# Optimization experiments

Hardware: AMD Instinct MI355X
Metric: run time of the kernel (lower is better)

## Reference

```python
import jax, jax.numpy as jnp
import numpy as np

T, B, H = 2048, 8, 1024


def setup_inputs() -> dict:
    key = jax.random.key(0)
    ks = jax.random.split(key, 4)
    scale = 1.0 / np.sqrt(H)
    x = jax.random.normal(ks[0], (T, B, H), dtype=jnp.float32)
    W_q = jax.random.normal(ks[1], (H, H), dtype=jnp.float32) * scale
    b_q = jnp.zeros((H,), dtype=jnp.float32)
    beta_raw = jax.random.normal(ks[2], (H,), dtype=jnp.float32)
    W_fc = jax.random.normal(ks[3], (H, H), dtype=jnp.float32) * scale
    b_fc = jnp.zeros((H,), dtype=jnp.float32)
    return {"x": x, "W_q": W_q, "b_q": b_q, "beta_raw": beta_raw,
            "W_fc": W_fc, "b_fc": b_fc}


def reference(x, W_q, b_q, beta_raw, W_fc, b_fc):
    # Per-neuron learned leak in (0,1)
    beta = jax.nn.sigmoid(beta_raw)  # (H,)
    # Input (q) projection: (T,B,H) @ (H,H)^T
    q = jnp.einsum('tbh,oh->tbo', x, W_q) + b_q  # (T,B,H)
    # Leaky integration m_t = beta * m_{t-1} + q_t as an associative scan over T
    a = jnp.broadcast_to(beta, q.shape)  # (T,B,H)

    def combine(c1, c2):
        a1, m1 = c1
        a2, m2 = c2
        return (a1 * a2, a2 * m1 + m2)

    _, m = jax.lax.associative_scan(combine, (a, q), axis=0)  # (T,B,H)
    # Linear + ReLU
    h = jnp.einsum('tbh,oh->tbo', m, W_fc) + b_fc
    return jax.nn.relu(h)
```

## Files before the change

kernel.cpp:

```cpp
#include <hip/hip_runtime.h>
#include <stdint.h>

typedef unsigned short u16;
typedef __bf16 bf16x8 __attribute__((ext_vector_type(8)));
typedef float f32x4 __attribute__((ext_vector_type(4)));

__device__ __forceinline__ u16 f2bf(float f) {
  union { float f; uint32_t u; } x; x.f = f;
  uint32_t u = x.u;
  u += 0x7fffu + ((u >> 16) & 1u);
  return (u16)(u >> 16);
}
__device__ __forceinline__ float bf2f(uint32_t lo16) {
  union { uint32_t u; float f; } x; x.u = lo16 << 16; return x.f;
}

__device__ __forceinline__ void async_load16(const u16* g, u16* l) {
  __builtin_amdgcn_global_load_lds(
      (const __attribute__((address_space(1))) void*)g,
      (__attribute__((address_space(3))) void*)l,
      16, 0, 0);
}

__global__ __launch_bounds__(256) void prep_all(const float* __restrict__ x,
                                                const float* __restrict__ Wq,
                                                const float* __restrict__ Wfc,
                                                const float* __restrict__ braw,
                                                u16* __restrict__ xb,
                                                u16* __restrict__ wqb,
                                                u16* __restrict__ wfcb,
                                                float* __restrict__ beta) {
  int gid = blockIdx.x * 256 + threadIdx.x;
  if (gid < 1024) beta[gid] = 1.0f / (1.0f + expf(-braw[gid]));
  if (gid < 131072) {
    const int HH = 1024 * 1024;
    int i = gid * 16;
    const float* src = (i < HH) ? (Wq + i) : (Wfc + (i - HH));
    u16* dst = (i < HH) ? (wqb + i) : (wfcb + (i - HH));
#pragma unroll
    for (int c = 0; c < 4; c++) {
      float4 v = *(const float4*)(src + c * 4);
      ushort4 o = {f2bf(v.x), f2bf(v.y), f2bf(v.z), f2bf(v.w)};
      *(ushort4*)(dst + c * 4) = o;
    }
  }
  {
    int i = gid * 8;
    float4 a = *(const float4*)(x + i);
    float4 b = *(const float4*)(x + i + 4);
    ushort4 o0 = {f2bf(a.x), f2bf(a.y), f2bf(a.z), f2bf(a.w)};
    ushort4 o1 = {f2bf(b.x), f2bf(b.y), f2bf(b.z), f2bf(b.w)};
    *(ushort4*)(xb + i) = o0;
    *(ushort4*)(xb + i + 4) = o1;
  }
}

template <int RELU, int OUTBF>
__global__ __launch_bounds__(256) void gemm_bt(const u16* __restrict__ A,
                                               const u16* __restrict__ B,
                                               const float* __restrict__ bias,
                                               void* __restrict__ Cout,
                                               int M, int N, int K) {
  __shared__ u16 As[128 * 32];
  __shared__ u16 Bs[128 * 32];

  const int tid  = threadIdx.x;
  const int lane = tid & 63;

  const int L  = blockIdx.x;
  const int xc = L & 7;
  const int k8 = L >> 3;
  const int tile_n = (k8 & 7) * 128;
  const int tile_m = ((xc << 4) | (k8 >> 3)) * 128;

  const int wm = ((tid >> 7) & 1) * 64;
  const int wn = ((tid >> 6) & 1) * 64;

  const int srow = tid >> 2;
  const int scol = (((tid & 3) ^ ((tid >> 3) & 3)) << 3);
  u16* ldsA = &As[(tid >> 6) << 9];
  u16* ldsB = &Bs[(tid >> 6) << 9];

  const u16* gA = A + (size_t)(tile_m + srow) * K + scol;
  const u16* gB = B + (size_t)(tile_n + srow) * K + scol;

  f32x4 acc[4][4];
#pragma unroll
  for (int i = 0; i < 4; i++)
#pragma unroll
    for (int j = 0; j < 4; j++) acc[i][j] = (f32x4){0.f, 0.f, 0.f, 0.f};

  const int lrow = lane & 15;
  const int gcq  = lane >> 4;
  const int ccL8 = (gcq ^ ((lrow >> 1) & 3)) << 3;

  for (int k0 = 0; k0 < K; k0 += 32) {
    __syncthreads();
    async_load16(gA + k0, ldsA);
    async_load16(gA + 64 * (size_t)K + k0, ldsA + 2048);
    async_load16(gB + k0, ldsB);
    async_load16(gB + 64 * (size_t)K + k0, ldsB + 2048);
    __builtin_amdgcn_s_waitcnt(0);
    __syncthreads();

    bf16x8 a[4], b[4];
#pragma unroll
    for (int i = 0; i < 4; i++)
      a[i] = *(const bf16x8*)&As[(wm + i * 16 + lrow) * 32 + ccL8];
#pragma unroll
    for (int j = 0; j < 4; j++)
      b[j] = *(const bf16x8*)&Bs[(wn + j * 16 + lrow) * 32 + ccL8];
#pragma unroll
    for (int i = 0; i < 4; i++)
#pragma unroll
      for (int j = 0; j < 4; j++)
        acc[i][j] = __builtin_amdgcn_mfma_f32_16x16x32_bf16(a[i], b[j], acc[i][j], 0, 0, 0);
  }

  const int crow = (lane >> 4) << 2;
  const int ccol = lane & 15;
#pragma unroll
  for (int i = 0; i < 4; i++) {
#pragma unroll
    for (int j = 0; j < 4; j++) {
      const int gm = tile_m + wm + i * 16 + crow;
      const int gn = tile_n + wn + j * 16 + ccol;
      const float bv = bias[gn];
#pragma unroll
      for (int r = 0; r < 4; r++) {
        float v = acc[i][j][r] + bv;
        if (RELU) v = fmaxf(v, 0.f);
        if (OUTBF) ((u16*)Cout)[(size_t)(gm + r) * N + gn] = f2bf(v);
        else       ((float*)Cout)[(size_t)(gm + r) * N + gn] = v;
      }
    }
  }
}

#define NCH 8192
#define SEG 32
#define NSEG 64

__global__ __launch_bounds__(256) void scan_carry(const uint2* __restrict__ qb,
                                                  float* __restrict__ carry,
                                                  const float* __restrict__ beta_arr) {
  int tid = blockIdx.x * 256 + threadIdx.x;
  int seg = tid >> 11;
  int cq  = tid & 2047;
  int h0  = (cq * 4) & 1023;
  float b0 = beta_arr[h0], b1 = beta_arr[h0 + 1], b2 = beta_arr[h0 + 2], b3 = beta_arr[h0 + 3];
  const uint2* p = qb + (size_t)seg * SEG * 2048 + cq;
  float m0 = 0.f, m1 = 0.f, m2 = 0.f, m3 = 0.f;
#pragma unroll 8
  for (int t = 0; t < SEG; t++) {
    uint2 v = p[(size_t)t * 2048];
    m0 = fmaf(b0, m0, bf2f(v.x & 0xffffu));
    m1 = fmaf(b1, m1, bf2f(v.x >> 16));
    m2 = fmaf(b2, m2, bf2f(v.y & 0xffffu));
    m3 = fmaf(b3, m3, bf2f(v.y >> 16));
  }
  *(float4*)&carry[(size_t)seg * NCH + cq * 4] = make_float4(m0, m1, m2, m3);
}

__global__ __launch_bounds__(256) void carry_scan(float* __restrict__ carry,
                                                  const float* __restrict__ beta_arr) {
  int ch = blockIdx.x * 256 + threadIdx.x;
  float beta = beta_arr[ch & 1023];
  float bseg = beta;
#pragma unroll
  for (int i = 0; i < 5; i++) bseg *= bseg;
  float c[NSEG];
#pragma unroll
  for (int s = 0; s < NSEG; s++) c[s] = carry[(size_t)s * NCH + ch];
  float F = 0.f;
#pragma unroll
  for (int s = 0; s < NSEG; s++) { float t = c[s]; c[s] = F; F = fmaf(bseg, F, t); }
#pragma unroll
  for (int s = 0; s < NSEG; s++) carry[(size_t)s * NCH + ch] = c[s];
}

__global__ __launch_bounds__(256) void scan_out(const uint2* __restrict__ qb,
                                                const float* __restrict__ carry,
                                                const float* __restrict__ beta_arr,
                                                uint2* __restrict__ mb) {
  int tid = blockIdx.x * 256 + threadIdx.x;
  int seg = tid >> 11;
  int cq  = tid & 2047;
  int h0  = (cq * 4) & 1023;
  float b0 = beta_arr[h0], b1 = beta_arr[h0 + 1], b2 = beta_arr[h0 + 2], b3 = beta_arr[h0 + 3];
  float4 F = *(const float4*)&carry[(size_t)seg * NCH + cq * 4];
  float m0 = F.x, m1 = F.y, m2 = F.z, m3 = F.w;
  const uint2* p = qb + (size_t)seg * SEG * 2048 + cq;
  uint2* o = mb + (size_t)seg * SEG * 2048 + cq;
#pragma unroll 8
  for (int t = 0; t < SEG; t++) {
    uint2 v = p[(size_t)t * 2048];
    m0 = fmaf(b0, m0, bf2f(v.x & 0xffffu));
    m1 = fmaf(b1, m1, bf2f(v.x >> 16));
    m2 = fmaf(b2, m2, bf2f(v.y & 0xffffu));
    m3 = fmaf(b3, m3, bf2f(v.y >> 16));
    uint2 w;
    w.x = (uint32_t)f2bf(m0) | ((uint32_t)f2bf(m1) << 16);
    w.y = (uint32_t)f2bf(m2) | ((uint32_t)f2bf(m3) << 16);
    o[(size_t)t * 2048] = w;
  }
}

extern "C" void kernel_launch(void* const* d_in, const int* in_sizes, int n_in,
                              void* d_out, int out_size, void* d_ws, size_t ws_size,
                              hipStream_t stream) {
  const float* x        = (const float*)d_in[0];
  const float* W_q      = (const float*)d_in[1];
  const float* b_q      = (const float*)d_in[2];
  const float* beta_raw = (const float*)d_in[3];
  const float* W_fc     = (const float*)d_in[4];
  const float* b_fc     = (const float*)d_in[5];

  const int H = 1024;
  const int M = 2048 * 8;
  const size_t MH = (size_t)M * H;

  char* ws = (char*)d_ws;
  u16* x_bf    = (u16*)ws;  ws += MH * 2;
  u16* q_bf    = (u16*)ws;  ws += MH * 2;
  u16* m_bf    = (u16*)ws;  ws += MH * 2;
  u16* wq_bf   = (u16*)ws;  ws += (size_t)H * H * 2;
  u16* wfc_bf  = (u16*)ws;  ws += (size_t)H * H * 2;
  float* beta  = (float*)ws; ws += 4096;
  float* carry = (float*)ws; ws += (size_t)NSEG * NCH * 4;

  prep_all<<<(int)(MH / 8 / 256), 256, 0, stream>>>(x, W_q, W_fc, beta_raw,
                                                    x_bf, wq_bf, wfc_bf, beta);

  gemm_bt<0, 1><<<1024, 256, 0, stream>>>(x_bf, wq_bf, b_q, q_bf, M, H, H);

  scan_carry<<<NSEG * (NCH / 4) / 256, 256, 0, stream>>>((const uint2*)q_bf, carry, beta);
  carry_scan<<<NCH / 256, 256, 0, stream>>>(carry, beta);
  scan_out<<<NSEG * (NCH / 4) / 256, 256, 0, stream>>>((const uint2*)q_bf, carry, beta,
                                                       (uint2*)m_bf);

  gemm_bt<1, 0><<<1024, 256, 0, stream>>>(m_bf, wfc_bf, b_fc, d_out, M, H, H);
}
```

Measured before the change: 263.7 us.

## Fuse per-tile scan carry into first GEMM epilogue and merge scan kernels

The q-projection GEMM now stages each output tile through LDS, writes it out with coalesced 16-byte stores, and computes per-segment scan carries (16 timesteps per 128-row tile) directly from the staged tile. The separate scan_carry and carry_scan kernels are removed; a single scan_fuse kernel recomputes the carry prefix serially over preceding segments and then does the local scan. This drops one full read of q and two launches, but adds LDS traffic and syncs to the GEMM epilogue and gives late segments a serial prefix loop of up to 127 steps.

After: 279.4 us. 6.0% more time.

```diff
diff --git a/kernel.cpp b/kernel.cpp
--- a/kernel.cpp
+++ b/kernel.cpp
@@ -59,6 +59,8 @@
 __global__ __launch_bounds__(256) void gemm_bt(const u16* __restrict__ A,
                                                const u16* __restrict__ B,
                                                const float* __restrict__ bias,
+                                               const float* __restrict__ beta_arr,
+                                               float* __restrict__ carry,
                                                void* __restrict__ Cout,
                                                int M, int N, int K) {
   __shared__ u16 As[128 * 32];
@@ -119,81 +121,101 @@
 
   const int crow = (lane >> 4) << 2;
   const int ccol = lane & 15;
-#pragma unroll
-  for (int i = 0; i < 4; i++) {
-#pragma unroll
-    for (int j = 0; j < 4; j++) {
-      const int gm = tile_m + wm + i * 16 + crow;
-      const int gn = tile_n + wn + j * 16 + ccol;
-      const float bv = bias[gn];
-#pragma unroll
-      for (int r = 0; r < 4; r++) {
-        float v = acc[i][j][r] + bv;
-        if (RELU) v = fmaxf(v, 0.f);
-        if (OUTBF) ((u16*)Cout)[(size_t)(gm + r) * N + gn] = f2bf(v);
-        else       ((float*)Cout)[(size_t)(gm + r) * N + gn] = v;
+
+  if (OUTBF) {
+    const int s = tile_m >> 7;
+    u16* Ct = As;
+    u16* qout = (u16*)Cout;
+#pragma unroll
+    for (int half = 0; half < 2; half++) {
+      __syncthreads();
+      if (wn == half * 64) {
+#pragma unroll
+        for (int i = 0; i < 4; i++)
+#pragma unroll
+          for (int j = 0; j < 4; j++) {
+            const int col = j * 16 + ccol;
+            const float bv = bias[tile_n + half * 64 + col];
+#pragma unroll
+            for (int r = 0; r < 4; r++) {
+              const int row = wm + i * 16 + crow + r;
+              const int cs = ((((col >> 3) ^ (row & 7)) << 3) | (col & 7));
+              float v = acc[i][j][r] + bv;
+              if (RELU) v = fmaxf(v, 0.f);
+              Ct[row * 64 + cs] = f2bf(v);
+            }
+          }
+      }
+      __syncthreads();
+      {
+        const int row = tid >> 1;
+        const int cb = (tid & 1) << 2;
+        u16* qr = qout + (size_t)(tile_m + row) * N + tile_n + half * 64;
+#pragma unroll
+        for (int k = 0; k < 4; k++) {
+          const int ck = (cb + k) ^ (row & 7);
+          *(uint4*)&qr[(cb + k) << 3] = *(const uint4*)&Ct[row * 64 + (ck << 3)];
+        }
+      }
+#pragma unroll
+      for (int cc = 0; cc < 2; cc++) {
+        const int c = tid + cc * 256;
+        const int b = c >> 6, hcol = c & 63;
+        const int h = tile_n + half * 64 + hcol;
+        const float bb = beta_arr[h];
+        float mloc = 0.f;
+#pragma unroll
+        for (int t = 0; t < 16; t++) {
+          const int cs = ((((hcol >> 3) ^ b) << 3) | (hcol & 7));
+          mloc = fmaf(bb, mloc, bf2f(Ct[(t * 8 + b) * 64 + cs]));
+        }
+        carry[(size_t)s * 8192 + b * 1024 + h] = mloc;
       }
     }
-  }
-}
-
-#define NCH 8192
-#define SEG 32
-#define NSEG 64
-
-__global__ __launch_bounds__(256) void scan_carry(const uint2* __restrict__ qb,
-                                                  float* __restrict__ carry,
-                                                  const float* __restrict__ beta_arr) {
-  int tid = blockIdx.x * 256 + threadIdx.x;
-  int seg = tid >> 11;
-  int cq  = tid & 2047;
-  int h0  = (cq * 4) & 1023;
-  float b0 = beta_arr[h0], b1 = beta_arr[h0 + 1], b2 = beta_arr[h0 + 2], b3 = beta_arr[h0 + 3];
-  const uint2* p = qb + (size_t)seg * SEG * 2048 + cq;
-  float m0 = 0.f, m1 = 0.f, m2 = 0.f, m3 = 0.f;
-#pragma unroll 8
-  for (int t = 0; t < SEG; t++) {
-    uint2 v = p[(size_t)t * 2048];
-    m0 = fmaf(b0, m0, bf2f(v.x & 0xffffu));
-    m1 = fmaf(b1, m1, bf2f(v.x >> 16));
-    m2 = fmaf(b2, m2, bf2f(v.y & 0xffffu));
-    m3 = fmaf(b3, m3, bf2f(v.y >> 16));
-  }
-  *(float4*)&carry[(size_t)seg * NCH + cq * 4] = make_float4(m0, m1, m2, m3);
-}
-
-__global__ __launch_bounds__(256) void carry_scan(float* __restrict__ carry,
-                                                  const float* __restrict__ beta_arr) {
-  int ch = blockIdx.x * 256 + threadIdx.x;
-  float beta = beta_arr[ch & 1023];
-  float bseg = beta;
-#pragma unroll
-  for (int i = 0; i < 5; i++) bseg *= bseg;
-  float c[NSEG];
-#pragma unroll
-  for (int s = 0; s < NSEG; s++) c[s] = carry[(size_t)s * NCH + ch];
-  float F = 0.f;
-#pragma unroll
-  for (int s = 0; s < NSEG; s++) { float t = c[s]; c[s] = F; F = fmaf(bseg, F, t); }
-#pragma unroll
-  for (int s = 0; s < NSEG; s++) carry[(size_t)s * NCH + ch] = c[s];
-}
-
-__global__ __launch_bounds__(256) void scan_out(const uint2* __restrict__ qb,
-                                                const float* __restrict__ carry,
-                                                const float* __restrict__ beta_arr,
-                                                uint2* __restrict__ mb) {
-  int tid = blockIdx.x * 256 + threadIdx.x;
-  int seg = tid >> 11;
-  int cq  = tid & 2047;
-  int h0  = (cq * 4) & 1023;
-  float b0 = beta_arr[h0], b1 = beta_arr[h0 + 1], b2 = beta_arr[h0 + 2], b3 = beta_arr[h0 + 3];
-  float4 F = *(const float4*)&carry[(size_t)seg * NCH + cq * 4];
-  float m0 = F.x, m1 = F.y, m2 = F.z, m3 = F.w;
-  const uint2* p = qb + (size_t)seg * SEG * 2048 + cq;
-  uint2* o = mb + (size_t)seg * SEG * 2048 + cq;
-#pragma unroll 8
-  for (int t = 0; t < SEG; t++) {
+  } else {
+#pragma unroll
+    for (int i = 0; i < 4; i++) {
+#pragma unroll
+      for (int j = 0; j < 4; j++) {
+        const int gm = tile_m + wm + i * 16 + crow;
+        const int gn = tile_n + wn + j * 16 + ccol;
+        const float bv = bias[gn];
+#pragma unroll
+        for (int r = 0; r < 4; r++) {
+          float v = acc[i][j][r] + bv;
+          if (RELU) v = fmaxf(v, 0.f);
+          ((float*)Cout)[(size_t)(gm + r) * N + gn] = v;
+        }
+      }
+    }
+  }
+}
+
+__global__ __launch_bounds__(256) void scan_fuse(const uint2* __restrict__ qb,
+                                                 const float4* __restrict__ carry4,
+                                                 const float* __restrict__ beta_arr,
+                                                 uint2* __restrict__ mb) {
+  const int tid = blockIdx.x * 256 + threadIdx.x;
+  const int seg = tid >> 11;
+  const int cq  = tid & 2047;
+  const int h0  = (cq * 4) & 1023;
+  const float b0 = beta_arr[h0], b1 = beta_arr[h0 + 1];
+  const float b2 = beta_arr[h0 + 2], b3 = beta_arr[h0 + 3];
+  float s0 = b0, s1 = b1, s2 = b2, s3 = b3;
+#pragma unroll
+  for (int i = 0; i < 4; i++) { s0 *= s0; s1 *= s1; s2 *= s2; s3 *= s3; }
+  float F0 = 0.f, F1 = 0.f, F2 = 0.f, F3 = 0.f;
+  const float4* cp = carry4 + cq;
+  for (int s = 0; s < seg; s++) {
+    float4 c = cp[(size_t)s * 2048];
+    F0 = fmaf(s0, F0, c.x); F1 = fmaf(s1, F1, c.y);
+    F2 = fmaf(s2, F2, c.z); F3 = fmaf(s3, F3, c.w);
+  }
+  const uint2* p = qb + (size_t)seg * 16 * 2048 + cq;
+  uint2* o = mb + (size_t)seg * 16 * 2048 + cq;
+  float m0 = F0, m1 = F1, m2 = F2, m3 = F3;
+#pragma unroll
+  for (int t = 0; t < 16; t++) {
     uint2 v = p[(size_t)t * 2048];
     m0 = fmaf(b0, m0, bf2f(v.x & 0xffffu));
     m1 = fmaf(b1, m1, bf2f(v.x >> 16));
@@ -227,17 +249,17 @@
   u16* wq_bf   = (u16*)ws;  ws += (size_t)H * H * 2;
   u16* wfc_bf  = (u16*)ws;  ws += (size_t)H * H * 2;
   float* beta  = (float*)ws; ws += 4096;
-  float* carry = (float*)ws; ws += (size_t)NSEG * NCH * 4;
+  float* carry = (float*)ws; ws += (size_t)128 * 8192 * 4;
 
   prep_all<<<(int)(MH / 8 / 256), 256, 0, stream>>>(x, W_q, W_fc, beta_raw,
                                                     x_bf, wq_bf, wfc_bf, beta);
 
-  gemm_bt<0, 1><<<1024, 256, 0, stream>>>(x_bf, wq_bf, b_q, q_bf, M, H, H);
-
-  scan_carry<<<NSEG * (NCH / 4) / 256, 256, 0, stream>>>((const uint2*)q_bf, carry, beta);
-  carry_scan<<<NCH / 256, 256, 0, stream>>>(carry, beta);
-  scan_out<<<NSEG * (NCH / 4) / 256, 256, 0, stream>>>((const uint2*)q_bf, carry, beta,
-                                                       (uint2*)m_bf);
-
-  gemm_bt<1, 0><<<1024, 256, 0, stream>>>(m_bf, wfc_bf, b_fc, d_out, M, H, H);
-}
+  gemm_bt<0, 1><<<1024, 256, 0, stream>>>(x_bf, wq_bf, b_q, beta, carry,
+                                          q_bf, M, H, H);
+
+  scan_fuse<<<1024, 256, 0, stream>>>((const uint2*)q_bf, (const float4*)carry,
+                                      beta, (uint2*)m_bf);
+
+  gemm_bt<1, 0><<<1024, 256, 0, stream>>>(m_bf, wfc_bf, b_fc, nullptr, nullptr,
+                                          d_out, M, H, H);
+}
```

## Double GEMM K-tile to 64 and fold carry scan into scan output kernel

Applied to the files above, without the earlier changes.

The GEMM now stages a 128x64 K-slice per iteration with an 8-way XOR swizzle, which halves the number of barrier and wait rounds per K loop and doubles the MFMA work between syncs. It also removes the separate carry_scan kernel. Each scan thread now rebuilds its incoming carry by serially folding the preceding segment sums, which saves one launch and one round trip through global memory. The cost is redundant carry work that grows with segment index, plus twice the LDS per GEMM block.

After: 251.9 us. 4.5% less time.

```diff
diff --git a/kernel.cpp b/kernel.cpp
--- a/kernel.cpp
+++ b/kernel.cpp
@@ -61,8 +61,8 @@
                                                const float* __restrict__ bias,
                                                void* __restrict__ Cout,
                                                int M, int N, int K) {
-  __shared__ u16 As[128 * 32];
-  __shared__ u16 Bs[128 * 32];
+  __shared__ u16 As[128 * 64];
+  __shared__ u16 Bs[128 * 64];
 
   const int tid  = threadIdx.x;
   const int lane = tid & 63;
@@ -76,13 +76,13 @@
   const int wm = ((tid >> 7) & 1) * 64;
   const int wn = ((tid >> 6) & 1) * 64;
 
-  const int srow = tid >> 2;
-  const int scol = (((tid & 3) ^ ((tid >> 3) & 3)) << 3);
-  u16* ldsA = &As[(tid >> 6) << 9];
-  u16* ldsB = &Bs[(tid >> 6) << 9];
-
-  const u16* gA = A + (size_t)(tile_m + srow) * K + scol;
-  const u16* gB = B + (size_t)(tile_n + srow) * K + scol;
+  const int srow   = tid >> 3;
+  const int schunk = (tid & 7) ^ ((tid >> 3) & 7);
+  u16* ldsA = &As[((tid >> 6) * 8) * 64];
+  u16* ldsB = &Bs[((tid >> 6) * 8) * 64];
+
+  const u16* gA = A + (size_t)(tile_m + srow) * K + schunk * 8;
+  const u16* gB = B + (size_t)(tile_n + srow) * K + schunk * 8;
 
   f32x4 acc[4][4];
 #pragma unroll
@@ -91,30 +91,34 @@
     for (int j = 0; j < 4; j++) acc[i][j] = (f32x4){0.f, 0.f, 0.f, 0.f};
 
   const int lrow = lane & 15;
-  const int gcq  = lane >> 4;
-  const int ccL8 = (gcq ^ ((lrow >> 1) & 3)) << 3;
-
-  for (int k0 = 0; k0 < K; k0 += 32) {
+  const int kq   = lane >> 4;
+
+  for (int k0 = 0; k0 < K; k0 += 64) {
     __syncthreads();
-    async_load16(gA + k0, ldsA);
-    async_load16(gA + 64 * (size_t)K + k0, ldsA + 2048);
-    async_load16(gB + k0, ldsB);
-    async_load16(gB + 64 * (size_t)K + k0, ldsB + 2048);
+#pragma unroll
+    for (int i = 0; i < 4; i++) {
+      async_load16(gA + (size_t)(i * 32) * K + k0, ldsA + i * 32 * 64);
+      async_load16(gB + (size_t)(i * 32) * K + k0, ldsB + i * 32 * 64);
+    }
     __builtin_amdgcn_s_waitcnt(0);
     __syncthreads();
 
-    bf16x8 a[4], b[4];
-#pragma unroll
-    for (int i = 0; i < 4; i++)
-      a[i] = *(const bf16x8*)&As[(wm + i * 16 + lrow) * 32 + ccL8];
-#pragma unroll
-    for (int j = 0; j < 4; j++)
-      b[j] = *(const bf16x8*)&Bs[(wn + j * 16 + lrow) * 32 + ccL8];
-#pragma unroll
-    for (int i = 0; i < 4; i++)
+#pragma unroll
+    for (int js = 0; js < 2; js++) {
+      const int cc = ((kq + 4 * js) ^ (lane & 7)) << 3;
+      bf16x8 a[4], b[4];
+#pragma unroll
+      for (int i = 0; i < 4; i++)
+        a[i] = *(const bf16x8*)&As[(wm + i * 16 + lrow) * 64 + cc];
 #pragma unroll
       for (int j = 0; j < 4; j++)
-        acc[i][j] = __builtin_amdgcn_mfma_f32_16x16x32_bf16(a[i], b[j], acc[i][j], 0, 0, 0);
+        b[j] = *(const bf16x8*)&Bs[(wn + j * 16 + lrow) * 64 + cc];
+#pragma unroll
+      for (int i = 0; i < 4; i++)
+#pragma unroll
+        for (int j = 0; j < 4; j++)
+          acc[i][j] = __builtin_amdgcn_mfma_f32_16x16x32_bf16(a[i], b[j], acc[i][j], 0, 0, 0);
+    }
   }
 
   const int crow = (lane >> 4) << 2;
@@ -162,34 +166,26 @@
   *(float4*)&carry[(size_t)seg * NCH + cq * 4] = make_float4(m0, m1, m2, m3);
 }
 
-__global__ __launch_bounds__(256) void carry_scan(float* __restrict__ carry,
-                                                  const float* __restrict__ beta_arr) {
-  int ch = blockIdx.x * 256 + threadIdx.x;
-  float beta = beta_arr[ch & 1023];
-  float bseg = beta;
-#pragma unroll
-  for (int i = 0; i < 5; i++) bseg *= bseg;
-  float c[NSEG];
-#pragma unroll
-  for (int s = 0; s < NSEG; s++) c[s] = carry[(size_t)s * NCH + ch];
-  float F = 0.f;
-#pragma unroll
-  for (int s = 0; s < NSEG; s++) { float t = c[s]; c[s] = F; F = fmaf(bseg, F, t); }
-#pragma unroll
-  for (int s = 0; s < NSEG; s++) carry[(size_t)s * NCH + ch] = c[s];
-}
-
-__global__ __launch_bounds__(256) void scan_out(const uint2* __restrict__ qb,
-                                                const float* __restrict__ carry,
-                                                const float* __restrict__ beta_arr,
-                                                uint2* __restrict__ mb) {
-  int tid = blockIdx.x * 256 + threadIdx.x;
-  int seg = tid >> 11;
-  int cq  = tid & 2047;
-  int h0  = (cq * 4) & 1023;
-  float b0 = beta_arr[h0], b1 = beta_arr[h0 + 1], b2 = beta_arr[h0 + 2], b3 = beta_arr[h0 + 3];
-  float4 F = *(const float4*)&carry[(size_t)seg * NCH + cq * 4];
-  float m0 = F.x, m1 = F.y, m2 = F.z, m3 = F.w;
+__global__ __launch_bounds__(256) void scan_fuse(const uint2* __restrict__ qb,
+                                                 const float4* __restrict__ carry4,
+                                                 const float* __restrict__ beta_arr,
+                                                 uint2* __restrict__ mb) {
+  const int tid = blockIdx.x * 256 + threadIdx.x;
+  const int seg = tid >> 11;
+  const int cq  = tid & 2047;
+  const int h0  = (cq * 4) & 1023;
+  const float b0 = beta_arr[h0], b1 = beta_arr[h0 + 1];
+  const float b2 = beta_arr[h0 + 2], b3 = beta_arr[h0 + 3];
+  float s0 = b0, s1 = b1, s2 = b2, s3 = b3;
+#pragma unroll
+  for (int i = 0; i < 5; i++) { s0 *= s0; s1 *= s1; s2 *= s2; s3 *= s3; }
+  float m0 = 0.f, m1 = 0.f, m2 = 0.f, m3 = 0.f;
+  const float4* cp = carry4 + cq;
+  for (int s = 0; s < seg; s++) {
+    float4 c = cp[(size_t)s * 2048];
+    m0 = fmaf(s0, m0, c.x); m1 = fmaf(s1, m1, c.y);
+    m2 = fmaf(s2, m2, c.z); m3 = fmaf(s3, m3, c.w);
+  }
   const uint2* p = qb + (size_t)seg * SEG * 2048 + cq;
   uint2* o = mb + (size_t)seg * SEG * 2048 + cq;
 #pragma unroll 8
@@ -235,9 +231,9 @@
   gemm_bt<0, 1><<<1024, 256, 0, stream>>>(x_bf, wq_bf, b_q, q_bf, M, H, H);
 
   scan_carry<<<NSEG * (NCH / 4) / 256, 256, 0, stream>>>((const uint2*)q_bf, carry, beta);
-  carry_scan<<<NCH / 256, 256, 0, stream>>>(carry, beta);
-  scan_out<<<NSEG * (NCH / 4) / 256, 256, 0, stream>>>((const uint2*)q_bf, carry, beta,
-                                                       (uint2*)m_bf);
+  scan_fuse<<<NSEG * (NCH / 4) / 256, 256, 0, stream>>>((const uint2*)q_bf,
+                                                        (const float4*)carry, beta,
+                                                        (uint2*)m_bf);
 
   gemm_bt<1, 0><<<1024, 256, 0, stream>>>(m_bf, wfc_bf, b_fc, d_out, M, H, H);
 }
```
